# Optimization experiments

Hardware: AMD Instinct MI355X
Metric: run time of the kernel (lower is better)

Reference implementation:

```python
import jax, jax.numpy as jnp
import numpy as np

NEG_SLOPE = 0.01  # F.leaky_relu default
BN_EPS = 1e-5


def _nnconv_bn_lrelu(x, src, dst, ef, W_edge, b_edge, W_root, b_root, gamma, beta):
    # PyG NNConv (aggr='add'): msg_e = x_src[e] @ reshape(nn(edge_feat[e]), [in, out])
    E = ef.shape[0]
    in_c = x.shape[1]
    out_c = W_root.shape[1]
    We = (ef @ W_edge.T + b_edge).reshape(E, in_c, out_c)   # [E, in, out]
    msg = jnp.einsum('ei,eio->eo', x[src], We)               # gather + per-edge matvec
    aggr = jax.ops.segment_sum(msg, dst, num_segments=x.shape[0])  # scatter-add
    h = aggr + x @ W_root + b_root
    # BatchNorm1d in training mode: batch statistics over nodes (biased var)
    mean = jnp.mean(h, axis=0)
    var = jnp.var(h, axis=0)
    hn = (h - mean) * jax.lax.rsqrt(var + BN_EPS) * gamma + beta
    return jnp.where(hn > 0, hn, NEG_SLOPE * hn)             # LeakyReLU


def setup_inputs() -> dict:
    key = jax.random.key(0)
    ks = jax.random.split(key, 12)
    N, E = 8192, 32768
    D_NODE, D_EDGE, H, OUT = 64, 64, 64, 128
    node_features = jax.random.normal(ks[0], (N, D_NODE), dtype=jnp.float32)
    edge_index = jax.random.randint(ks[1], (2, E), 0, N, dtype=jnp.int32)
    edge_features = jax.random.normal(ks[2], (E, D_EDGE), dtype=jnp.float32)
    batch = jnp.zeros((N,), dtype=jnp.int32)
    s = 0.05
    params = {
        # layer 0: node_feats=D_NODE, edge_feats=D_EDGE, out=H
        'W_edge0': jax.random.normal(ks[3], (D_NODE * H, D_EDGE), dtype=jnp.float32) * s,
        'b_edge0': jnp.zeros((D_NODE * H,), dtype=jnp.float32),
        'W_root0': jax.random.normal(ks[4], (D_NODE, H), dtype=jnp.float32) * s,
        'b_root0': jnp.zeros((H,), dtype=jnp.float32),
        'gamma0': jnp.ones((H,), dtype=jnp.float32),
        'beta0': jnp.zeros((H,), dtype=jnp.float32),
        # layer 1: node_feats=H, edge_feats=H(==D_EDGE), out=H
        'W_edge1': jax.random.normal(ks[5], (H * H, D_EDGE), dtype=jnp.float32) * s,
        'b_edge1': jnp.zeros((H * H,), dtype=jnp.float32),
        'W_root1': jax.random.normal(ks[6], (H, H), dtype=jnp.float32) * s,
        'b_root1': jnp.zeros((H,), dtype=jnp.float32),
        'gamma1': jnp.ones((H,), dtype=jnp.float32),
        'beta1': jnp.zeros((H,), dtype=jnp.float32),
        # final linear
        'W_lin': jax.random.normal(ks[7], (OUT, H), dtype=jnp.float32) * s,
        'b_lin': jnp.zeros((OUT,), dtype=jnp.float32),
    }
    return {'node_features': node_features, 'edge_index': edge_index,
            'edge_features': edge_features, 'batch': batch, **params}


def reference(node_features, edge_index, edge_features, batch,
              W_edge0, b_edge0, W_root0, b_root0, gamma0, beta0,
              W_edge1, b_edge1, W_root1, b_root1, gamma1, beta1,
              W_lin, b_lin):
    src, dst = edge_index[0], edge_index[1]
    h = _nnconv_bn_lrelu(node_features, src, dst, edge_features,
                         W_edge0, b_edge0, W_root0, b_root0, gamma0, beta0)
    h = _nnconv_bn_lrelu(h, src, dst, edge_features,
                         W_edge1, b_edge1, W_root1, b_root1, gamma1, beta1)
    # dropout treated as identity (eval-mode determinism)
    return h @ W_lin.T + b_lin
```

## Files before the change

### kernel.cpp

```cpp
#include <hip/hip_runtime.h>

typedef __bf16 bf16x8 __attribute__((ext_vector_type(8)));
typedef float f32x4 __attribute__((ext_vector_type(4)));

#define NEG_SLOPE 0.01f
#define BN_EPS 1e-5f

static __device__ __forceinline__ unsigned short f2bf(float f) {
    unsigned u = __builtin_bit_cast(unsigned, f);
    unsigned r = (u + 0x7fffu + ((u >> 16) & 1u)) >> 16;
    return (unsigned short)r;
}
static __device__ __forceinline__ float lrelu(float v) {
    return fmaxf(v, 0.f) + NEG_SLOPE * fminf(v, 0.f);
}
static __device__ __forceinline__ f32x4 bn4(f32x4 v, f32x4 sc, f32x4 sh) {
    f32x4 r = v * sc + sh;
    r.x = lrelu(r.x); r.y = lrelu(r.y); r.z = lrelu(r.z); r.w = lrelu(r.w);
    return r;
}

__global__ __launch_bounds__(256) void prep(const float* __restrict__ We0,
                                            const float* __restrict__ We1,
                                            unsigned short* __restrict__ wbs0,
                                            unsigned short* __restrict__ wbs1,
                                            float* __restrict__ stats,
                                            int* __restrict__ counters,
                                            const int* __restrict__ dst,
                                            int* __restrict__ hist, int E) {
    const int idx = blockIdx.x * 256 + threadIdx.x;
    if (blockIdx.x == 0) {
        stats[threadIdx.x] = 0.f;
        if (threadIdx.x < 2) counters[threadIdx.x] = 0;
    }
    if (idx < 65536) {
        const int t = idx;
        const float* We = (t >> 15) ? We1 : We0;
        unsigned short* wbs = (t >> 15) ? wbs1 : wbs0;
        const int r = t & 32767;
        const int i = r >> 9, os = (r >> 7) & 3, h = (r >> 6) & 1, l = r & 63;
        const float* sp = We + (size_t)(i * 64 + 16 * os + (l & 15)) * 64
                             + h * 32 + 8 * (l >> 4);
        const f32x4 v0 = *reinterpret_cast<const f32x4*>(sp);
        const f32x4 v1 = *reinterpret_cast<const f32x4*>(sp + 4);
        ushort4 u0, u1;
        u0.x = f2bf(v0.x); u0.y = f2bf(v0.y); u0.z = f2bf(v0.z); u0.w = f2bf(v0.w);
        u1.x = f2bf(v1.x); u1.y = f2bf(v1.y); u1.z = f2bf(v1.z); u1.w = f2bf(v1.w);
        *reinterpret_cast<ushort4*>(wbs + (size_t)r * 8) = u0;
        *reinterpret_cast<ushort4*>(wbs + (size_t)r * 8 + 4) = u1;
    } else {
        const int e = idx - 65536;
        if (e < E) atomicAdd(&hist[dst[e]], 1);
    }
}

__global__ __launch_bounds__(256) void scan_kernel(const int* __restrict__ hist,
                                                   int* __restrict__ ofs,
                                                   int* __restrict__ cur, int N) {
    __shared__ int wsum[4];
    const int tid = threadIdx.x;
    const int per = N / 256;
    const int base = tid * per;
    int loc[32];
    int s = 0;
#pragma unroll
    for (int k = 0; k < 32; ++k) { loc[k] = s; s += hist[base + k]; }
    const int lane = tid & 63, w = tid >> 6;
    int run = s;
#pragma unroll
    for (int d = 1; d < 64; d <<= 1) {
        int up = __shfl_up(run, d, 64);
        if (lane >= d) run += up;
    }
    const int excl = run - s;
    if (lane == 63) wsum[w] = run;
    __syncthreads();
    int woff = 0;
#pragma unroll
    for (int i = 0; i < 4; ++i) woff += (i < w) ? wsum[i] : 0;
    if (tid == 255) ofs[N] = woff + run;
    const int off = woff + excl;
#pragma unroll
    for (int k = 0; k < 32; ++k) {
        ofs[base + k] = off + loc[k];
        cur[base + k] = off + loc[k];
    }
}

__global__ __launch_bounds__(256) void scatter_reorder(
    const int* __restrict__ dst, const int* __restrict__ src,
    const float* __restrict__ ef, int* __restrict__ cur,
    unsigned short* __restrict__ ef_bs, int* __restrict__ src_s) {
    const int e = blockIdx.x * 256 + threadIdx.x;
    const int p = atomicAdd(&cur[dst[e]], 1);
    src_s[p] = src[e];
    const float* er = ef + (size_t)e * 64;
    unsigned short* orow = ef_bs + (size_t)p * 64;
#pragma unroll
    for (int c = 0; c < 16; ++c) {
        const f32x4 v = *reinterpret_cast<const f32x4*>(er + 4 * c);
        ushort4 u;
        u.x = f2bf(v.x); u.y = f2bf(v.y); u.z = f2bf(v.z); u.w = f2bf(v.w);
        *reinterpret_cast<ushort4*>(orow + 4 * c) = u;
    }
}

__global__ __launch_bounds__(256) void node_mm2(const float* __restrict__ x,
                                                const float* __restrict__ Wr,
                                                const float* __restrict__ br,
                                                float* __restrict__ aggr,
                                                const float* __restrict__ be,
                                                float* __restrict__ NB,
                                                const float* __restrict__ ss) {
    const float* M; const float* bias; float* out;
    if (blockIdx.y == 0) { M = Wr; bias = br; out = aggr; }
    else                 { M = be; bias = nullptr; out = NB; }
    __shared__ float Ml[64][64];
    __shared__ float xl[64][64];
    const int tid = threadIdx.x;
    const int n0 = blockIdx.x * 64;
    for (int f = tid; f < 1024; f += 256) {
        int r = f >> 4, c = f & 15;
        *reinterpret_cast<float4*>(&Ml[r][c * 4]) =
            *reinterpret_cast<const float4*>(M + (size_t)r * 64 + c * 4);
        f32x4 xv = *reinterpret_cast<const f32x4*>(x + (size_t)(n0 + r) * 64 + c * 4);
        if (ss) {
            const f32x4 sc = *reinterpret_cast<const f32x4*>(ss + c * 4);
            const f32x4 sh = *reinterpret_cast<const f32x4*>(ss + 64 + c * 4);
            xv = bn4(xv, sc, sh);
        }
        *reinterpret_cast<f32x4*>(&xl[r][c * 4]) = xv;
    }
    __syncthreads();
    const int o = tid & 63, g = tid >> 6;
    float acc[16] = {};
    for (int i4 = 0; i4 < 16; ++i4) {
        float m0 = Ml[4 * i4 + 0][o], m1 = Ml[4 * i4 + 1][o];
        float m2 = Ml[4 * i4 + 2][o], m3 = Ml[4 * i4 + 3][o];
#pragma unroll
        for (int k = 0; k < 16; ++k) {
            const f32x4 xv = *reinterpret_cast<const f32x4*>(&xl[g + 4 * k][4 * i4]);
            acc[k] += xv.x * m0 + xv.y * m1 + xv.z * m2 + xv.w * m3;
        }
    }
    const float b = bias ? bias[o] : 0.f;
#pragma unroll
    for (int k = 0; k < 16; ++k)
        out[(size_t)(n0 + g + 4 * k) * 64 + o] = acc[k] + b;
}

__global__ __launch_bounds__(512, 1) void msg_fused(
    const unsigned short* __restrict__ ef_bs,
    const unsigned short* __restrict__ wbs,
    const float* __restrict__ x,
    const float* __restrict__ NB,
    const int* __restrict__ src_s,
    float* __restrict__ msg,
    const float* __restrict__ ss) {
    __shared__ unsigned short wlds[32768];
    __shared__ float xT2[8192];
    const int tid = threadIdx.x;
    const int e0 = blockIdx.x * 128;

#pragma unroll
    for (int it = 0; it < 4; ++it) {
        int f = it * 512 + tid;
        int e = f & 127, c = f >> 7;
        int s = src_s[e0 + e];
        f32x4 xv = *reinterpret_cast<const f32x4*>(x + (size_t)s * 64 + c * 4);
        if (ss) {
            const f32x4 sc = *reinterpret_cast<const f32x4*>(ss + c * 4);
            const f32x4 sh = *reinterpret_cast<const f32x4*>(ss + 64 + c * 4);
            xv = bn4(xv, sc, sh);
        }
        const int eln = e & 15, ehh = e >> 4;
        xT2[(4 * c + 0) * 128 + eln * 8 + ehh] = xv.x;
        xT2[(4 * c + 1) * 128 + eln * 8 + ehh] = xv.y;
        xT2[(4 * c + 2) * 128 + eln * 8 + ehh] = xv.z;
        xT2[(4 * c + 3) * 128 + eln * 8 + ehh] = xv.w;
    }

    const int w = tid >> 6, l = tid & 63, lg = l >> 4, ln = l & 15;
    const int os = w & 3, eh = w >> 2;

    bf16x8 B0[4], B1[4];
#pragma unroll
    for (int tt = 0; tt < 4; ++tt) {
        const unsigned short* pe = ef_bs + (size_t)(e0 + 64 * eh + 16 * tt + ln) * 64 + 8 * lg;
        B0[tt] = *reinterpret_cast<const bf16x8*>(pe);
        B1[tt] = *reinterpret_cast<const bf16x8*>(pe + 32);
    }

    const char* gW = (const char*)wbs;
    char* wldsB = (char*)wlds;
#define GLD(c, j) (*reinterpret_cast<const bf16x8*>(gW + (size_t)(c) * 65536 + (j) * 8192 + tid * 16))
#define SST(j, v) (*reinterpret_cast<bf16x8*>(wldsB + (j) * 8192 + tid * 16) = (v))

    bf16x8 S0 = GLD(0, 0), S1 = GLD(0, 1), S2 = GLD(0, 2), S3 = GLD(0, 3);
    bf16x8 S4 = GLD(0, 4), S5 = GLD(0, 5), S6 = GLD(0, 6), S7 = GLD(0, 7);
    SST(0, S0); SST(1, S1); SST(2, S2); SST(3, S3);
    SST(4, S4); SST(5, S5); SST(6, S6); SST(7, S7);
    S0 = GLD(1, 0); S1 = GLD(1, 1); S2 = GLD(1, 2); S3 = GLD(1, 3);
    S4 = GLD(1, 4); S5 = GLD(1, 5); S6 = GLD(1, 6); S7 = GLD(1, 7);
    __syncthreads();

    f32x4 acc[4] = {};
    const unsigned short* wb_ = wlds + os * 1024 + l * 8;
    for (int t = 0; t < 8; ++t) {
#pragma unroll
        for (int ii = 0; ii < 8; ++ii) {
            const bf16x8 A0 = *reinterpret_cast<const bf16x8*>(wb_ + ii * 4096);
            const bf16x8 A1 = *reinterpret_cast<const bf16x8*>(wb_ + ii * 4096 + 512);
            const f32x4 xs = *reinterpret_cast<const f32x4*>(
                &xT2[(t * 8 + ii) * 128 + ln * 8 + eh * 4]);
#pragma unroll
            for (int tt = 0; tt < 4; ++tt) {
                f32x4 c = {};
                c = __builtin_amdgcn_mfma_f32_16x16x32_bf16(A0, B0[tt], c, 0, 0, 0);
                c = __builtin_amdgcn_mfma_f32_16x16x32_bf16(A1, B1[tt], c, 0, 0, 0);
                acc[tt] += xs[tt] * c;
            }
        }
        __syncthreads();
        if (t < 7) {
            SST(0, S0); SST(1, S1); SST(2, S2); SST(3, S3);
            SST(4, S4); SST(5, S5); SST(6, S6); SST(7, S7);
            if (t < 6) {
                S0 = GLD(t + 2, 0); S1 = GLD(t + 2, 1);
                S2 = GLD(t + 2, 2); S3 = GLD(t + 2, 3);
                S4 = GLD(t + 2, 4); S5 = GLD(t + 2, 5);
                S6 = GLD(t + 2, 6); S7 = GLD(t + 2, 7);
            }
            __syncthreads();
        }
    }
#undef GLD
#undef SST

#pragma unroll
    for (int tt = 0; tt < 4; ++tt) {
        const int e = e0 + 64 * eh + 16 * tt + ln;
        const int s = src_s[e];
        const f32x4 nbv = *reinterpret_cast<const f32x4*>(NB + (size_t)s * 64 + os * 16 + 4 * lg);
        const f32x4 add = acc[tt] + nbv;
        *reinterpret_cast<f32x4*>(msg + (size_t)e * 64 + os * 16 + 4 * lg) = add;
    }
}

__global__ __launch_bounds__(256) void gather_k(const float* __restrict__ msg,
                                                const int* __restrict__ ofs,
                                                float* __restrict__ aggr) {
    const int tid = threadIdx.x;
    const int w = tid >> 6, lane = tid & 63;
    const int v = blockIdx.x * 4 + w;
    const int beg = ofs[v], end = ofs[v + 1];
    float a0 = 0.f, a1 = 0.f, a2 = 0.f, a3 = 0.f;
    int j = beg;
    for (; j + 4 <= end; j += 4) {
        a0 += msg[(size_t)(j + 0) * 64 + lane];
        a1 += msg[(size_t)(j + 1) * 64 + lane];
        a2 += msg[(size_t)(j + 2) * 64 + lane];
        a3 += msg[(size_t)(j + 3) * 64 + lane];
    }
    for (; j < end; ++j) a0 += msg[(size_t)j * 64 + lane];
    aggr[(size_t)v * 64 + lane] += (a0 + a1) + (a2 + a3);
}

__global__ __launch_bounds__(256) void bn_stats(const float* __restrict__ h,
                                                float* __restrict__ sums,
                                                const float* __restrict__ gamma,
                                                const float* __restrict__ beta,
                                                float* __restrict__ ss,
                                                float invN,
                                                int* __restrict__ counter,
                                                int nblk) {
    const int tid = threadIdx.x;
    const int o = tid & 63, g = tid >> 6;
    const int n0 = blockIdx.x * 128;
    float s = 0.f, s2 = 0.f;
    for (int k = 0; k < 32; ++k) {
        float v = h[(size_t)(n0 + g * 32 + k) * 64 + o];
        s += v; s2 += v * v;
    }
    __shared__ float red[2][4][64];
    __shared__ int lastFlag;
    red[0][g][o] = s; red[1][g][o] = s2;
    __syncthreads();
    if (g == 0) {
        s  = red[0][0][o] + red[0][1][o] + red[0][2][o] + red[0][3][o];
        s2 = red[1][0][o] + red[1][1][o] + red[1][2][o] + red[1][3][o];
        atomicAdd(&sums[o], s);
        atomicAdd(&sums[64 + o], s2);
    }
    __threadfence();
    __syncthreads();
    if (tid == 0) lastFlag = (atomicAdd(counter, 1) == nblk - 1);
    __syncthreads();
    if (lastFlag && tid < 64) {
        const float sv  = atomicAdd(&sums[tid], 0.f);
        const float sv2 = atomicAdd(&sums[64 + tid], 0.f);
        const float mean = sv * invN;
        const float var  = sv2 * invN - mean * mean;
        const float sc = gamma[tid] * rsqrtf(var + BN_EPS);
        ss[tid] = sc;
        ss[64 + tid] = beta[tid] - mean * sc;
    }
}

__global__ __launch_bounds__(256) void out_kernel(const float* __restrict__ x2,
                                                  const float* __restrict__ Wl,
                                                  const float* __restrict__ bl,
                                                  float* __restrict__ out,
                                                  const float* __restrict__ ss) {
    __shared__ float Wt[64][129];
    __shared__ float xl[64][64];
    const int tid = threadIdx.x;
    const int n0 = blockIdx.x * 64;
    for (int f = tid; f < 8192; f += 256) {
        int q = f >> 6, o = f & 63;
        Wt[o][q] = Wl[f];
    }
    for (int f = tid; f < 1024; f += 256) {
        int r = f >> 4, c = f & 15;
        f32x4 xv = *reinterpret_cast<const f32x4*>(x2 + (size_t)(n0 + r) * 64 + c * 4);
        const f32x4 sc = *reinterpret_cast<const f32x4*>(ss + c * 4);
        const f32x4 sh = *reinterpret_cast<const f32x4*>(ss + 64 + c * 4);
        xv = bn4(xv, sc, sh);
        *reinterpret_cast<f32x4*>(&xl[r][c * 4]) = xv;
    }
    __syncthreads();
    const int q = tid & 127, ng = tid >> 7;
    float acc[32] = {};
    for (int o4 = 0; o4 < 16; ++o4) {
        float w0 = Wt[4 * o4 + 0][q], w1 = Wt[4 * o4 + 1][q];
        float w2 = Wt[4 * o4 + 2][q], w3 = Wt[4 * o4 + 3][q];
#pragma unroll
        for (int k = 0; k < 32; ++k) {
            const f32x4 xv = *reinterpret_cast<const f32x4*>(&xl[ng + 2 * k][4 * o4]);
            acc[k] += xv.x * w0 + xv.y * w1 + xv.z * w2 + xv.w * w3;
        }
    }
    const float b = bl[q];
#pragma unroll
    for (int k = 0; k < 32; ++k)
        out[(size_t)(n0 + ng + 2 * k) * 128 + q] = acc[k] + b;
}

extern "C" void kernel_launch(void* const* d_in, const int* in_sizes, int n_in,
                              void* d_out, int out_size, void* d_ws, size_t ws_size,
                              hipStream_t stream) {
    const float* nf      = (const float*)d_in[0];
    const int*   ei      = (const int*)d_in[1];
    const float* ef      = (const float*)d_in[2];
    const float* W_edge0 = (const float*)d_in[4];
    const float* b_edge0 = (const float*)d_in[5];
    const float* W_root0 = (const float*)d_in[6];
    const float* b_root0 = (const float*)d_in[7];
    const float* gamma0  = (const float*)d_in[8];
    const float* beta0   = (const float*)d_in[9];
    const float* W_edge1 = (const float*)d_in[10];
    const float* b_edge1 = (const float*)d_in[11];
    const float* W_root1 = (const float*)d_in[12];
    const float* b_root1 = (const float*)d_in[13];
    const float* gamma1  = (const float*)d_in[14];
    const float* beta1   = (const float*)d_in[15];
    const float* W_lin   = (const float*)d_in[16];
    const float* b_lin   = (const float*)d_in[17];

    const int N = in_sizes[0] / 64;
    const int E = in_sizes[1] / 2;
    const int* src = ei;
    const int* dst = ei + E;

    unsigned short* ef_bs = (unsigned short*)d_ws;
    unsigned short* wbs0  = ef_bs + (size_t)E * 64;
    unsigned short* wbs1  = wbs0 + 262144;
    float* msg   = (float*)(wbs1 + 262144);
    float* aggr0 = msg + (size_t)E * 64;
    float* aggr1 = aggr0 + (size_t)N * 64;
    float* NBbuf = aggr1 + (size_t)N * 64;
    float* stats = NBbuf + (size_t)N * 64;
    float* ssbuf = stats + 256;
    int*   cnt   = (int*)(ssbuf + 256);
    int*   hist  = cnt + 2;
    int*   ofs   = hist + N;
    int*   cur   = ofs + N + 1;
    int*   src_s = cur + N;

    const float invN = 1.0f / (float)N;

    hipMemsetAsync(hist, 0, N * sizeof(int), stream);
    prep<<<(65536 + E) / 256, 256, 0, stream>>>(W_edge0, W_edge1, wbs0, wbs1,
                                                stats, cnt, dst, hist, E);
    scan_kernel<<<1, 256, 0, stream>>>(hist, ofs, cur, N);
    scatter_reorder<<<E / 256, 256, 0, stream>>>(dst, src, ef, cur, ef_bs, src_s);

    node_mm2<<<dim3(N / 64, 2), 256, 0, stream>>>(nf, W_root0, b_root0, aggr0,
                                                  b_edge0, NBbuf, nullptr);
    msg_fused<<<E / 128, 512, 0, stream>>>(ef_bs, wbs0, nf, NBbuf, src_s, msg, nullptr);
    gather_k<<<N / 4, 256, 0, stream>>>(msg, ofs, aggr0);
    bn_stats<<<N / 128, 256, 0, stream>>>(aggr0, stats, gamma0, beta0, ssbuf,
                                          invN, cnt + 0, N / 128);

    node_mm2<<<dim3(N / 64, 2), 256, 0, stream>>>(aggr0, W_root1, b_root1, aggr1,
                                                  b_edge1, NBbuf, ssbuf);
    msg_fused<<<E / 128, 512, 0, stream>>>(ef_bs, wbs1, aggr0, NBbuf, src_s, msg, ssbuf);
    gather_k<<<N / 4, 256, 0, stream>>>(msg, ofs, aggr1);
    bn_stats<<<N / 128, 256, 0, stream>>>(aggr1, stats + 128, gamma1, beta1, ssbuf + 128,
                                          invN, cnt + 1, N / 128);

    out_kernel<<<N / 64, 256, 0, stream>>>(aggr1, W_lin, b_lin, (float*)d_out, ssbuf + 128);
}
```

Baseline: 144.5 us.

## Fuse BN stats into gather, merge node matmuls, halve msg LDS stage for occupancy

Folds batch-norm statistic accumulation into the gather/scatter-add kernel via per-block atomics, removing the separate bn_stats kernels and their completion counters. The scale/shift finalisation is recomputed per block in the consumer kernels. node_mm2 now computes the root and edge-bias products in one launch, sharing the x tile. msg_fused stages half as much weight data in LDS per step with twice as many steps and raises launch bounds to 2 blocks per CU for more overlap. The cost is more synchronisation steps in msg_fused and some redundant per-block BN finalisation.

```diff
diff --git a/kernel.cpp b/kernel.cpp
--- a/kernel.cpp
+++ b/kernel.cpp
@@ -25,14 +25,10 @@
                                             unsigned short* __restrict__ wbs0,
                                             unsigned short* __restrict__ wbs1,
                                             float* __restrict__ stats,
-                                            int* __restrict__ counters,
                                             const int* __restrict__ dst,
                                             int* __restrict__ hist, int E) {
     const int idx = blockIdx.x * 256 + threadIdx.x;
-    if (blockIdx.x == 0) {
-        stats[threadIdx.x] = 0.f;
-        if (threadIdx.x < 2) counters[threadIdx.x] = 0;
-    }
+    if (blockIdx.x == 0) stats[threadIdx.x] = 0.f;
     if (idx < 65536) {
         const int t = idx;
         const float* We = (t >> 15) ? We1 : We0;
@@ -105,62 +101,90 @@
     }
 }
 
-__global__ __launch_bounds__(256) void node_mm2(const float* __restrict__ x,
-                                                const float* __restrict__ Wr,
-                                                const float* __restrict__ br,
-                                                float* __restrict__ aggr,
-                                                const float* __restrict__ be,
-                                                float* __restrict__ NB,
-                                                const float* __restrict__ ss) {
-    const float* M; const float* bias; float* out;
-    if (blockIdx.y == 0) { M = Wr; bias = br; out = aggr; }
-    else                 { M = be; bias = nullptr; out = NB; }
+__global__ __launch_bounds__(256) void node_mm2(
+    const float* __restrict__ x,
+    const float* __restrict__ Wr, const float* __restrict__ br,
+    const float* __restrict__ be,
+    float* __restrict__ aggr, float* __restrict__ NB,
+    const float* __restrict__ sums, const float* __restrict__ gamma,
+    const float* __restrict__ beta, float invN) {
     __shared__ float Ml[64][64];
+    __shared__ float Bl[64][64];
     __shared__ float xl[64][64];
+    __shared__ float ssl[128];
     const int tid = threadIdx.x;
+    if (sums) {
+        if (tid < 64) {
+            const float mean = sums[tid] * invN;
+            const float var  = sums[64 + tid] * invN - mean * mean;
+            const float sc = gamma[tid] * rsqrtf(var + BN_EPS);
+            ssl[tid] = sc;
+            ssl[64 + tid] = beta[tid] - mean * sc;
+        }
+        __syncthreads();
+    }
     const int n0 = blockIdx.x * 64;
     for (int f = tid; f < 1024; f += 256) {
         int r = f >> 4, c = f & 15;
         *reinterpret_cast<float4*>(&Ml[r][c * 4]) =
-            *reinterpret_cast<const float4*>(M + (size_t)r * 64 + c * 4);
+            *reinterpret_cast<const float4*>(Wr + (size_t)r * 64 + c * 4);
+        *reinterpret_cast<float4*>(&Bl[r][c * 4]) =
+            *reinterpret_cast<const float4*>(be + (size_t)r * 64 + c * 4);
         f32x4 xv = *reinterpret_cast<const f32x4*>(x + (size_t)(n0 + r) * 64 + c * 4);
-        if (ss) {
-            const f32x4 sc = *reinterpret_cast<const f32x4*>(ss + c * 4);
-            const f32x4 sh = *reinterpret_cast<const f32x4*>(ss + 64 + c * 4);
+        if (sums) {
+            const f32x4 sc = *reinterpret_cast<const f32x4*>(&ssl[c * 4]);
+            const f32x4 sh = *reinterpret_cast<const f32x4*>(&ssl[64 + c * 4]);
             xv = bn4(xv, sc, sh);
         }
         *reinterpret_cast<f32x4*>(&xl[r][c * 4]) = xv;
     }
     __syncthreads();
     const int o = tid & 63, g = tid >> 6;
-    float acc[16] = {};
+    float accA[16] = {}, accB[16] = {};
     for (int i4 = 0; i4 < 16; ++i4) {
         float m0 = Ml[4 * i4 + 0][o], m1 = Ml[4 * i4 + 1][o];
         float m2 = Ml[4 * i4 + 2][o], m3 = Ml[4 * i4 + 3][o];
+        float b0 = Bl[4 * i4 + 0][o], b1 = Bl[4 * i4 + 1][o];
+        float b2 = Bl[4 * i4 + 2][o], b3 = Bl[4 * i4 + 3][o];
 #pragma unroll
         for (int k = 0; k < 16; ++k) {
             const f32x4 xv = *reinterpret_cast<const f32x4*>(&xl[g + 4 * k][4 * i4]);
-            acc[k] += xv.x * m0 + xv.y * m1 + xv.z * m2 + xv.w * m3;
-        }
-    }
-    const float b = bias ? bias[o] : 0.f;
-#pragma unroll
-    for (int k = 0; k < 16; ++k)
-        out[(size_t)(n0 + g + 4 * k) * 64 + o] = acc[k] + b;
-}
-
-__global__ __launch_bounds__(512, 1) void msg_fused(
+            accA[k] += xv.x * m0 + xv.y * m1 + xv.z * m2 + xv.w * m3;
+            accB[k] += xv.x * b0 + xv.y * b1 + xv.z * b2 + xv.w * b3;
+        }
+    }
+    const float b = br[o];
+#pragma unroll
+    for (int k = 0; k < 16; ++k) {
+        aggr[(size_t)(n0 + g + 4 * k) * 64 + o] = accA[k] + b;
+        NB[(size_t)(n0 + g + 4 * k) * 64 + o]   = accB[k];
+    }
+}
+
+__global__ __launch_bounds__(512, 2) void msg_fused(
     const unsigned short* __restrict__ ef_bs,
     const unsigned short* __restrict__ wbs,
     const float* __restrict__ x,
     const float* __restrict__ NB,
     const int* __restrict__ src_s,
     float* __restrict__ msg,
-    const float* __restrict__ ss) {
-    __shared__ unsigned short wlds[32768];
+    const float* __restrict__ sums, const float* __restrict__ gamma,
+    const float* __restrict__ beta, float invN) {
+    __shared__ unsigned short wlds[16384];
     __shared__ float xT2[8192];
+    __shared__ float ssl[128];
     const int tid = threadIdx.x;
     const int e0 = blockIdx.x * 128;
+    if (sums) {
+        if (tid < 64) {
+            const float mean = sums[tid] * invN;
+            const float var  = sums[64 + tid] * invN - mean * mean;
+            const float sc = gamma[tid] * rsqrtf(var + BN_EPS);
+            ssl[tid] = sc;
+            ssl[64 + tid] = beta[tid] - mean * sc;
+        }
+        __syncthreads();
+    }
 
 #pragma unroll
     for (int it = 0; it < 4; ++it) {
@@ -168,9 +192,9 @@
         int e = f & 127, c = f >> 7;
         int s = src_s[e0 + e];
         f32x4 xv = *reinterpret_cast<const f32x4*>(x + (size_t)s * 64 + c * 4);
-        if (ss) {
-            const f32x4 sc = *reinterpret_cast<const f32x4*>(ss + c * 4);
-            const f32x4 sh = *reinterpret_cast<const f32x4*>(ss + 64 + c * 4);
+        if (sums) {
+            const f32x4 sc = *reinterpret_cast<const f32x4*>(&ssl[c * 4]);
+            const f32x4 sh = *reinterpret_cast<const f32x4*>(&ssl[64 + c * 4]);
             xv = bn4(xv, sc, sh);
         }
         const int eln = e & 15, ehh = e >> 4;
@@ -193,26 +217,23 @@
 
     const char* gW = (const char*)wbs;
     char* wldsB = (char*)wlds;
-#define GLD(c, j) (*reinterpret_cast<const bf16x8*>(gW + (size_t)(c) * 65536 + (j) * 8192 + tid * 16))
+#define GLD(c, j) (*reinterpret_cast<const bf16x8*>(gW + (size_t)(c) * 32768 + (j) * 8192 + tid * 16))
 #define SST(j, v) (*reinterpret_cast<bf16x8*>(wldsB + (j) * 8192 + tid * 16) = (v))
 
     bf16x8 S0 = GLD(0, 0), S1 = GLD(0, 1), S2 = GLD(0, 2), S3 = GLD(0, 3);
-    bf16x8 S4 = GLD(0, 4), S5 = GLD(0, 5), S6 = GLD(0, 6), S7 = GLD(0, 7);
     SST(0, S0); SST(1, S1); SST(2, S2); SST(3, S3);
-    SST(4, S4); SST(5, S5); SST(6, S6); SST(7, S7);
     S0 = GLD(1, 0); S1 = GLD(1, 1); S2 = GLD(1, 2); S3 = GLD(1, 3);
-    S4 = GLD(1, 4); S5 = GLD(1, 5); S6 = GLD(1, 6); S7 = GLD(1, 7);
     __syncthreads();
 
     f32x4 acc[4] = {};
     const unsigned short* wb_ = wlds + os * 1024 + l * 8;
-    for (int t = 0; t < 8; ++t) {
-#pragma unroll
-        for (int ii = 0; ii < 8; ++ii) {
+    for (int t = 0; t < 16; ++t) {
+#pragma unroll
+        for (int ii = 0; ii < 4; ++ii) {
             const bf16x8 A0 = *reinterpret_cast<const bf16x8*>(wb_ + ii * 4096);
             const bf16x8 A1 = *reinterpret_cast<const bf16x8*>(wb_ + ii * 4096 + 512);
             const f32x4 xs = *reinterpret_cast<const f32x4*>(
-                &xT2[(t * 8 + ii) * 128 + ln * 8 + eh * 4]);
+                &xT2[(t * 4 + ii) * 128 + ln * 8 + eh * 4]);
 #pragma unroll
             for (int tt = 0; tt < 4; ++tt) {
                 f32x4 c = {};
@@ -222,14 +243,11 @@
             }
         }
         __syncthreads();
-        if (t < 7) {
+        if (t < 15) {
             SST(0, S0); SST(1, S1); SST(2, S2); SST(3, S3);
-            SST(4, S4); SST(5, S5); SST(6, S6); SST(7, S7);
-            if (t < 6) {
+            if (t < 14) {
                 S0 = GLD(t + 2, 0); S1 = GLD(t + 2, 1);
                 S2 = GLD(t + 2, 2); S3 = GLD(t + 2, 3);
-                S4 = GLD(t + 2, 4); S5 = GLD(t + 2, 5);
-                S6 = GLD(t + 2, 6); S7 = GLD(t + 2, 7);
             }
             __syncthreads();
         }
@@ -247,9 +265,10 @@
     }
 }
 
-__global__ __launch_bounds__(256) void gather_k(const float* __restrict__ msg,
-                                                const int* __restrict__ ofs,
-                                                float* __restrict__ aggr) {
+__global__ __launch_bounds__(256) void gather_bn2(const float* __restrict__ msg,
+                                                  const int* __restrict__ ofs,
+                                                  float* __restrict__ aggr,
+                                                  float* __restrict__ stats) {
     const int tid = threadIdx.x;
     const int w = tid >> 6, lane = tid & 63;
     const int v = blockIdx.x * 4 + w;
@@ -263,58 +282,37 @@
         a3 += msg[(size_t)(j + 3) * 64 + lane];
     }
     for (; j < end; ++j) a0 += msg[(size_t)j * 64 + lane];
-    aggr[(size_t)v * 64 + lane] += (a0 + a1) + (a2 + a3);
-}
-
-__global__ __launch_bounds__(256) void bn_stats(const float* __restrict__ h,
-                                                float* __restrict__ sums,
-                                                const float* __restrict__ gamma,
-                                                const float* __restrict__ beta,
-                                                float* __restrict__ ss,
-                                                float invN,
-                                                int* __restrict__ counter,
-                                                int nblk) {
-    const int tid = threadIdx.x;
-    const int o = tid & 63, g = tid >> 6;
-    const int n0 = blockIdx.x * 128;
-    float s = 0.f, s2 = 0.f;
-    for (int k = 0; k < 32; ++k) {
-        float v = h[(size_t)(n0 + g * 32 + k) * 64 + o];
-        s += v; s2 += v * v;
-    }
+    const float val = aggr[(size_t)v * 64 + lane] + (a0 + a1) + (a2 + a3);
+    aggr[(size_t)v * 64 + lane] = val;
+
     __shared__ float red[2][4][64];
-    __shared__ int lastFlag;
-    red[0][g][o] = s; red[1][g][o] = s2;
-    __syncthreads();
-    if (g == 0) {
-        s  = red[0][0][o] + red[0][1][o] + red[0][2][o] + red[0][3][o];
-        s2 = red[1][0][o] + red[1][1][o] + red[1][2][o] + red[1][3][o];
-        atomicAdd(&sums[o], s);
-        atomicAdd(&sums[64 + o], s2);
-    }
-    __threadfence();
-    __syncthreads();
-    if (tid == 0) lastFlag = (atomicAdd(counter, 1) == nblk - 1);
-    __syncthreads();
-    if (lastFlag && tid < 64) {
-        const float sv  = atomicAdd(&sums[tid], 0.f);
-        const float sv2 = atomicAdd(&sums[64 + tid], 0.f);
-        const float mean = sv * invN;
-        const float var  = sv2 * invN - mean * mean;
-        const float sc = gamma[tid] * rsqrtf(var + BN_EPS);
-        ss[tid] = sc;
-        ss[64 + tid] = beta[tid] - mean * sc;
-    }
-}
-
-__global__ __launch_bounds__(256) void out_kernel(const float* __restrict__ x2,
-                                                  const float* __restrict__ Wl,
-                                                  const float* __restrict__ bl,
-                                                  float* __restrict__ out,
-                                                  const float* __restrict__ ss) {
+    red[0][w][lane] = val; red[1][w][lane] = val * val;
+    __syncthreads();
+    if (w == 0) {
+        const float s  = red[0][0][lane] + red[0][1][lane] + red[0][2][lane] + red[0][3][lane];
+        const float s2 = red[1][0][lane] + red[1][1][lane] + red[1][2][lane] + red[1][3][lane];
+        atomicAdd(&stats[lane], s);
+        atomicAdd(&stats[64 + lane], s2);
+    }
+}
+
+__global__ __launch_bounds__(256) void out_kernel(
+    const float* __restrict__ x2, const float* __restrict__ Wl,
+    const float* __restrict__ bl, float* __restrict__ out,
+    const float* __restrict__ sums, const float* __restrict__ gamma,
+    const float* __restrict__ beta, float invN) {
     __shared__ float Wt[64][129];
     __shared__ float xl[64][64];
+    __shared__ float ssl[128];
     const int tid = threadIdx.x;
+    if (tid < 64) {
+        const float mean = sums[tid] * invN;
+        const float var  = sums[64 + tid] * invN - mean * mean;
+        const float sc = gamma[tid] * rsqrtf(var + BN_EPS);
+        ssl[tid] = sc;
+        ssl[64 + tid] = beta[tid] - mean * sc;
+    }
+    __syncthreads();
     const int n0 = blockIdx.x * 64;
     for (int f = tid; f < 8192; f += 256) {
         int q = f >> 6, o = f & 63;
@@ -323,8 +321,8 @@
     for (int f = tid; f < 1024; f += 256) {
         int r = f >> 4, c = f & 15;
         f32x4 xv = *reinterpret_cast<const f32x4*>(x2 + (size_t)(n0 + r) * 64 + c * 4);
-        const f32x4 sc = *reinterpret_cast<const f32x4*>(ss + c * 4);
-        const f32x4 sh = *reinterpret_cast<const f32x4*>(ss + 64 + c * 4);
+        const f32x4 sc = *reinterpret_cast<const f32x4*>(&ssl[c * 4]);
+        const f32x4 sh = *reinterpret_cast<const f32x4*>(&ssl[64 + c * 4]);
         xv = bn4(xv, sc, sh);
         *reinterpret_cast<f32x4*>(&xl[r][c * 4]) = xv;
     }
@@ -380,9 +378,7 @@
     float* aggr1 = aggr0 + (size_t)N * 64;
     float* NBbuf = aggr1 + (size_t)N * 64;
     float* stats = NBbuf + (size_t)N * 64;
-    float* ssbuf = stats + 256;
-    int*   cnt   = (int*)(ssbuf + 256);
-    int*   hist  = cnt + 2;
+    int*   hist  = (int*)(stats + 256);
     int*   ofs   = hist + N;
     int*   cur   = ofs + N + 1;
     int*   src_s = cur + N;
@@ -391,23 +387,22 @@
 
     hipMemsetAsync(hist, 0, N * sizeof(int), stream);
     prep<<<(65536 + E) / 256, 256, 0, stream>>>(W_edge0, W_edge1, wbs0, wbs1,
-                                                stats, cnt, dst, hist, E);
+                                                stats, dst, hist, E);
     scan_kernel<<<1, 256, 0, stream>>>(hist, ofs, cur, N);
     scatter_reorder<<<E / 256, 256, 0, stream>>>(dst, src, ef, cur, ef_bs, src_s);
 
-    node_mm2<<<dim3(N / 64, 2), 256, 0, stream>>>(nf, W_root0, b_root0, aggr0,
-                                                  b_edge0, NBbuf, nullptr);
-    msg_fused<<<E / 128, 512, 0, stream>>>(ef_bs, wbs0, nf, NBbuf, src_s, msg, nullptr);
-    gather_k<<<N / 4, 256, 0, stream>>>(msg, ofs, aggr0);
-    bn_stats<<<N / 128, 256, 0, stream>>>(aggr0, stats, gamma0, beta0, ssbuf,
-                                          invN, cnt + 0, N / 128);
-
-    node_mm2<<<dim3(N / 64, 2), 256, 0, stream>>>(aggr0, W_root1, b_root1, aggr1,
-                                                  b_edge1, NBbuf, ssbuf);
-    msg_fused<<<E / 128, 512, 0, stream>>>(ef_bs, wbs1, aggr0, NBbuf, src_s, msg, ssbuf);
-    gather_k<<<N / 4, 256, 0, stream>>>(msg, ofs, aggr1);
-    bn_stats<<<N / 128, 256, 0, stream>>>(aggr1, stats + 128, gamma1, beta1, ssbuf + 128,
-                                          invN, cnt + 1, N / 128);
-
-    out_kernel<<<N / 64, 256, 0, stream>>>(aggr1, W_lin, b_lin, (float*)d_out, ssbuf + 128);
-}
+    node_mm2<<<N / 64, 256, 0, stream>>>(nf, W_root0, b_root0, b_edge0, aggr0, NBbuf,
+                                         nullptr, nullptr, nullptr, invN);
+    msg_fused<<<E / 128, 512, 0, stream>>>(ef_bs, wbs0, nf, NBbuf, src_s, msg,
+                                           nullptr, nullptr, nullptr, invN);
+    gather_bn2<<<N / 4, 256, 0, stream>>>(msg, ofs, aggr0, stats);
+
+    node_mm2<<<N / 64, 256, 0, stream>>>(aggr0, W_root1, b_root1, b_edge1, aggr1, NBbuf,
+                                         stats, gamma0, beta0, invN);
+    msg_fused<<<E / 128, 512, 0, stream>>>(ef_bs, wbs1, aggr0, NBbuf, src_s, msg,
+                                           stats, gamma0, beta0, invN);
+    gather_bn2<<<N / 4, 256, 0, stream>>>(msg, ofs, aggr1, stats + 128);
+
+    out_kernel<<<N / 64, 256, 0, stream>>>(aggr1, W_lin, b_lin, (float*)d_out,
+                                           stats + 128, gamma1, beta1, invN);
+}
```

Result: slower. 223.8 us (+54.9%).
